# Optimization experiments

Hardware: AMD Instinct MI355X
Metric: run time of the kernel (lower is better)

The kernel has to match this reference:

```python
import jax, jax.numpy as jnp
import numpy as np

D_MODEL = 1024
D_K = 1024
B = 4
T = 2048

def setup_inputs() -> dict:
    key = jax.random.key(0)
    k_x, k_q, k_k, k_v = jax.random.split(key, 4)
    s = 1.0 / np.sqrt(D_MODEL)
    return {
        "x": jax.random.normal(k_x, (B, T, D_MODEL), dtype=jnp.float32),
        "Wq": jax.random.normal(k_q, (D_MODEL, D_K), dtype=jnp.float32) * s,
        "Wk": jax.random.normal(k_k, (D_MODEL, D_K), dtype=jnp.float32) * s,
        "Wv": jax.random.normal(k_v, (D_MODEL, D_K), dtype=jnp.float32) * s,
    }

def reference(x, Wq, Wk, Wv):
    # x: (B, T, d_model); Wq/Wk/Wv: (d_model, d_k)
    Q = jnp.einsum('btd,dk->btk', x, Wq)
    K = jnp.einsum('btd,dk->btk', x, Wk)
    V = jnp.einsum('btd,dk->btk', x, Wv)
    scale = 1.0 / jnp.sqrt(jnp.asarray(D_K, dtype=x.dtype))
    scores = jnp.einsum('bqk,bsk->bqs', Q, K) * scale  # (B, T, T)
    t = scores.shape[1]
    causal = jnp.triu(jnp.ones((t, t), dtype=bool), k=1)  # True above diagonal
    scores = jnp.where(causal[None, :, :], jnp.asarray(-jnp.inf, dtype=scores.dtype), scores)
    weights = jax.nn.softmax(scores, axis=-1)
    # dropout p=0.0 -> identity
    return jnp.einsum('bqs,bsk->bqk', weights, V)
```

## Files before the change

kernel.cpp:

```cpp
#include <hip/hip_runtime.h>
#include <cstdint>

typedef __attribute__((ext_vector_type(4))) float f32x4;
typedef __attribute__((ext_vector_type(8))) __bf16 bf16x8;
typedef __attribute__((ext_vector_type(8))) unsigned short u16x8;

__device__ __forceinline__ unsigned short f2bf(float f) {
    union { float f; unsigned u; } v; v.f = f;
    unsigned u = v.u + 0x7FFFu + ((v.u >> 16) & 1u);
    return (unsigned short)(u >> 16);
}
__device__ __forceinline__ float bf2f(unsigned short h) {
    union { unsigned u; float f; } v; v.u = ((unsigned)h) << 16;
    return v.f;
}

__device__ __forceinline__ void gld_lds16(const void* g, void* l) {
    auto gp = reinterpret_cast<const __attribute__((address_space(1))) unsigned int*>(
        reinterpret_cast<uintptr_t>(g));
    auto lp = reinterpret_cast<__attribute__((address_space(3))) unsigned int*>(
        reinterpret_cast<uintptr_t>(l));
    __builtin_amdgcn_global_load_lds(gp, lp, 16, 0, 0);
}

template<int BF16OUT>
__device__ __forceinline__ void gemm8(
    const unsigned short* __restrict__ A, int lda,
    const unsigned short* __restrict__ B, int ldb,
    void* __restrict__ C, int ldc,
    int ktiles,
    unsigned short* lA, unsigned short* lB)
{
    const int t = threadIdx.x;
    const int l = t & 63;
    const int w = t >> 6;
    const int wr = w >> 1, wc = w & 1;

    f32x4 acc[2][4];
#pragma unroll
    for (int i = 0; i < 2; ++i)
#pragma unroll
        for (int j = 0; j < 4; ++j)
#pragma unroll
            for (int e = 0; e < 4; ++e) acc[i][j][e] = 0.f;

    auto stage = [&](int p, int kt) {
        const int k0 = kt << 6;
#pragma unroll
        for (int i = 0; i < 2; ++i) {
            const int flat = t + (i << 9);
            const int row = flat >> 3;
            const int sc = (flat & 7) ^ (row & 7);
            gld_lds16(A + (size_t)row * lda + k0 + (sc << 3), lA + (p << 13) + (flat << 3));
            gld_lds16(B + (size_t)row * ldb + k0 + (sc << 3), lB + (p << 13) + (flat << 3));
        }
    };

    auto compute = [&](int p) {
#pragma unroll
        for (int kk = 0; kk < 2; ++kk) {
            bf16x8 af[2], bfr[4];
            const int c = (kk << 5) + ((l >> 4) << 3);
#pragma unroll
            for (int mf = 0; mf < 2; ++mf) {
                const int r = (wr << 5) + (mf << 4) + (l & 15);
                const int ad = (((r << 6) + c) ^ ((r & 7) << 3)) + (p << 13);
                af[mf] = *(const bf16x8*)(lA + ad);
            }
#pragma unroll
            for (int nf = 0; nf < 4; ++nf) {
                const int r = (wc << 6) + (nf << 4) + (l & 15);
                const int ad = (((r << 6) + c) ^ ((r & 7) << 3)) + (p << 13);
                bfr[nf] = *(const bf16x8*)(lB + ad);
            }
            __builtin_amdgcn_s_setprio(1);
#pragma unroll
            for (int mf = 0; mf < 2; ++mf)
#pragma unroll
                for (int nf = 0; nf < 4; ++nf)
                    acc[mf][nf] = __builtin_amdgcn_mfma_f32_16x16x32_bf16(
                        af[mf], bfr[nf], acc[mf][nf], 0, 0, 0);
            __builtin_amdgcn_s_setprio(0);
        }
    };

    stage(0, 0);
    __syncthreads();
    int p = 0;
    for (int kt = 0; kt < ktiles - 1; ++kt) {
        stage(p ^ 1, kt + 1);
        compute(p);
        __syncthreads();
        p ^= 1;
    }
    compute(p);

#pragma unroll
    for (int mf = 0; mf < 2; ++mf)
#pragma unroll
        for (int nf = 0; nf < 4; ++nf)
#pragma unroll
            for (int j = 0; j < 4; ++j) {
                const int row = (wr << 5) + (mf << 4) + ((l >> 4) << 2) + j;
                const int col = (wc << 6) + (nf << 4) + (l & 15);
                const float v = acc[mf][nf][j];
                if (BF16OUT)
                    ((unsigned short*)C)[(size_t)row * ldc + col] = f2bf(v);
                else
                    ((float*)C)[(size_t)row * ldc + col] = v;
            }
}

__global__ __launch_bounds__(512, 4) void k_gemm_qk(
    const unsigned short* __restrict__ xb, const unsigned short* __restrict__ wtqk,
    unsigned short* __restrict__ qk)
{
    __shared__ unsigned short lA[16384], lB[16384];
    gemm8<1>(xb + (size_t)blockIdx.y * 128 * 1024, 1024,
             wtqk + (size_t)blockIdx.x * 128 * 1024, 1024,
             qk + (size_t)blockIdx.y * 128 * 2048 + blockIdx.x * 128, 2048,
             16, lA, lB);
}

__global__ __launch_bounds__(512, 4) void k_gemm_vt(
    const unsigned short* __restrict__ wtv, const unsigned short* __restrict__ xb,
    unsigned short* __restrict__ vt)
{
    __shared__ unsigned short lA[16384], lB[16384];
    gemm8<1>(wtv + (size_t)blockIdx.y * 128 * 1024, 1024,
             xb + (size_t)blockIdx.x * 128 * 1024, 1024,
             vt + (size_t)blockIdx.y * 128 * 8192 + blockIdx.x * 128, 8192,
             16, lA, lB);
}

__global__ __launch_bounds__(512, 4) void k_scores(
    const unsigned short* __restrict__ qk, unsigned short* __restrict__ S)
{
    const int kt = blockIdx.x, qt = blockIdx.y, b = blockIdx.z;
    if (kt > qt) return;
    __shared__ unsigned short lA[16384], lB[16384];
    gemm8<1>(qk + ((size_t)b * 2048 + qt * 128) * 2048, 2048,
             qk + ((size_t)b * 2048 + kt * 128) * 2048 + 1024, 2048,
             S + (size_t)b * 4194304 + (size_t)qt * 128 * 2048 + kt * 128, 2048,
             16, lA, lB);
}

__global__ __launch_bounds__(512, 4) void k_pv(
    const unsigned short* __restrict__ P, const unsigned short* __restrict__ Vt,
    float* __restrict__ out)
{
    const int dn = blockIdx.x, pr = blockIdx.y, b = blockIdx.z;
    __shared__ unsigned short lA[16384], lB[16384];
    const int q1 = pr, q2 = 15 - pr;
    gemm8<0>(P + (size_t)b * 4194304 + (size_t)q1 * 128 * 2048, 2048,
             Vt + (size_t)dn * 128 * 8192 + b * 2048, 8192,
             out + ((size_t)b * 2048 + q1 * 128) * 1024 + dn * 128, 1024,
             (q1 + 1) * 2, lA, lB);
    __syncthreads();
    gemm8<0>(P + (size_t)b * 4194304 + (size_t)q2 * 128 * 2048, 2048,
             Vt + (size_t)dn * 128 * 8192 + b * 2048, 8192,
             out + ((size_t)b * 2048 + q2 * 128) * 1024 + dn * 128, 1024,
             (q2 + 1) * 2, lA, lB);
}

__global__ __launch_bounds__(256) void k_cast_bf16(
    const float* __restrict__ in, unsigned short* __restrict__ out, int n8)
{
    const int i = blockIdx.x * 256 + threadIdx.x;
    if (i >= n8) return;
    const float4* p = (const float4*)in + (size_t)i * 2;
    const float4 a = p[0], b = p[1];
    u16x8 r;
    r[0] = f2bf(a.x); r[1] = f2bf(a.y); r[2] = f2bf(a.z); r[3] = f2bf(a.w);
    r[4] = f2bf(b.x); r[5] = f2bf(b.y); r[6] = f2bf(b.z); r[7] = f2bf(b.w);
    *(u16x8*)(out + (size_t)i * 8) = r;
}

__global__ __launch_bounds__(256) void k_transpose3(
    const float* __restrict__ Wq, const float* __restrict__ Wk, const float* __restrict__ Wv,
    unsigned short* __restrict__ wtqk, unsigned short* __restrict__ wtv)
{
    __shared__ float tile[32][33];
    const int z = blockIdx.z;
    const float* in = (z == 0) ? Wq : (z == 1) ? Wk : Wv;
    unsigned short* out = (z < 2) ? (wtqk + (size_t)z * 1048576) : wtv;
    const float s = (z == 0) ? 0.03125f : 1.0f;
    const int bx = blockIdx.x * 32, by = blockIdx.y * 32;
    const int tx = threadIdx.x, ty = threadIdx.y;
    for (int r = ty; r < 32; r += 8)
        tile[r][tx] = in[(size_t)(by + r) * 1024 + bx + tx];
    __syncthreads();
    for (int r = ty; r < 32; r += 8)
        out[(size_t)(bx + r) * 1024 + by + tx] = f2bf(tile[tx][r] * s);
}

__global__ __launch_bounds__(256) void k_softmax(unsigned short* __restrict__ S)
{
    const int w = threadIdx.x >> 6, l = threadIdx.x & 63;
    const int r = blockIdx.x * 4 + w;
    const int b = r >> 11, lr = r & 2047;
    unsigned short* row = S + ((size_t)b << 22) + ((size_t)lr << 11);
    const int edge = ((lr >> 7) + 1) << 7;

    float v[32];
#pragma unroll
    for (int i = 0; i < 4; ++i) {
        const int c0 = (l << 3) + (i << 9);
        if (c0 < edge) {
            const u16x8 u = *(const u16x8*)(row + c0);
#pragma unroll
            for (int j = 0; j < 8; ++j)
                v[(i << 3) + j] = (c0 + j <= lr) ? bf2f(u[j]) : -3.0e38f;
        } else {
#pragma unroll
            for (int j = 0; j < 8; ++j) v[(i << 3) + j] = -3.0e38f;
        }
    }
    float m = v[0];
#pragma unroll
    for (int k = 1; k < 32; ++k) m = fmaxf(m, v[k]);
#pragma unroll
    for (int s = 32; s; s >>= 1) m = fmaxf(m, __shfl_xor(m, s, 64));
    float sum = 0.f;
#pragma unroll
    for (int k = 0; k < 32; ++k) { const float e = __expf(v[k] - m); v[k] = e; sum += e; }
#pragma unroll
    for (int s = 32; s; s >>= 1) sum += __shfl_xor(sum, s, 64);
    const float inv = 1.f / sum;
#pragma unroll
    for (int i = 0; i < 4; ++i) {
        const int c0 = (l << 3) + (i << 9);
        if (c0 < edge) {
            u16x8 o;
#pragma unroll
            for (int j = 0; j < 8; ++j) o[j] = f2bf(v[(i << 3) + j] * inv);
            *(u16x8*)(row + c0) = o;
        }
    }
}

extern "C" void kernel_launch(void* const* d_in, const int* in_sizes, int n_in,
                              void* d_out, int out_size, void* d_ws, size_t ws_size,
                              hipStream_t stream)
{
    (void)in_sizes; (void)n_in; (void)out_size; (void)ws_size;
    const float* x  = (const float*)d_in[0];
    const float* Wq = (const float*)d_in[1];
    const float* Wk = (const float*)d_in[2];
    const float* Wv = (const float*)d_in[3];
    float* out = (float*)d_out;

    char* w = (char*)d_ws;
    unsigned short* xb   = (unsigned short*)(w);
    unsigned short* wtqk = (unsigned short*)(w + 16777216);
    unsigned short* wtv  = (unsigned short*)(w + 20971520);
    unsigned short* QK   = (unsigned short*)(w + 23068672);
    unsigned short* Vt   = (unsigned short*)(w + 56623104);
    unsigned short* S    = (unsigned short*)(w + 73400320);

    k_cast_bf16<<<4096, 256, 0, stream>>>(x, xb, 1048576);
    k_transpose3<<<dim3(32, 32, 3), dim3(32, 8), 0, stream>>>(Wq, Wk, Wv, wtqk, wtv);

    k_gemm_qk<<<dim3(16, 64), 512, 0, stream>>>(xb, wtqk, QK);
    k_gemm_vt<<<dim3(64, 8), 512, 0, stream>>>(wtv, xb, Vt);

    k_scores <<<dim3(16, 16, 4), 512, 0, stream>>>(QK, S);
    k_softmax<<<2048, 256, 0, stream>>>(S);
    k_pv     <<<dim3(8, 8, 4), 512, 0, stream>>>(S, Vt, out);
}
```

Measured before the change: 228.8 us.

## Use 256x256 tiled GEMM with phased pipeline for projections and scores

Adds a 256x256-tile GEMM with 8 waves, each computing 128x64. It uses double-buffered LDS staged in halves and interleaves loads with MFMA phases separated by barriers. The Q/K and V^T projections are merged into one launch with an XCD-aware block remap. The causal scores kernel now launches only the lower-triangle 256-tiles instead of early-exiting blocks. The larger tiles cut global traffic per FLOP and launch overhead, at the cost of fewer blocks, lower occupancy (launch bound 2) and more register pressure from 32 accumulators.

```diff
diff --git a/kernel.cpp b/kernel.cpp
--- a/kernel.cpp
+++ b/kernel.cpp
@@ -21,6 +21,131 @@
     auto lp = reinterpret_cast<__attribute__((address_space(3))) unsigned int*>(
         reinterpret_cast<uintptr_t>(l));
     __builtin_amdgcn_global_load_lds(gp, lp, 16, 0, 0);
+}
+
+#define MFMA_BF16(a, b, c) __builtin_amdgcn_mfma_f32_16x16x32_bf16((a), (b), (c), 0, 0, 0)
+
+template<int BF16OUT>
+__device__ __forceinline__ void gemm256(
+    const unsigned short* __restrict__ A, int lda,
+    const unsigned short* __restrict__ B, int ldb,
+    void* __restrict__ C, int ldc,
+    int ktiles,
+    unsigned short* lA, unsigned short* lB)
+{
+    const int t = threadIdx.x;
+    const int l = t & 63;
+    const int w = t >> 6;
+    const int wm = w >> 2, wn = w & 3;
+
+    f32x4 acc[8][4];
+#pragma unroll
+    for (int i = 0; i < 8; ++i)
+#pragma unroll
+        for (int j = 0; j < 4; ++j)
+#pragma unroll
+            for (int e = 0; e < 4; ++e) acc[i][j][e] = 0.f;
+
+    auto stage = [&](const unsigned short* __restrict__ G, int ld, unsigned short* L,
+                     int p, int h, int kt) {
+        const int k0 = kt << 6;
+#pragma unroll
+        for (int i = 0; i < 2; ++i) {
+            const int flat = t + (i << 9);
+            const int row  = (h << 7) + (flat >> 3);
+            const int sc   = (flat & 7) ^ (row & 7);
+            gld_lds16(G + (size_t)row * ld + k0 + (sc << 3),
+                      L + (p << 14) + (h << 13) + (flat << 3));
+        }
+    };
+
+    auto rdA = [&](int p, int mf, int kk) -> bf16x8 {
+        const int r = (wm << 7) + (mf << 4) + (l & 15);
+        const int c = (kk << 5) + ((l >> 4) << 3);
+        const int ad = (((r << 6) + c) ^ ((r & 7) << 3)) + (p << 14);
+        return *(const bf16x8*)(lA + ad);
+    };
+    auto rdB = [&](int p, int nf, int kk) -> bf16x8 {
+        const int r = (wn << 6) + (nf << 4) + (l & 15);
+        const int c = (kk << 5) + ((l >> 4) << 3);
+        const int ad = (((r << 6) + c) ^ ((r & 7) << 3)) + (p << 14);
+        return *(const bf16x8*)(lB + ad);
+    };
+
+    const int kt1 = (ktiles > 1) ? 1 : 0;
+    stage(B, ldb, lB, 0, 0, 0); stage(B, ldb, lB, 0, 1, 0);
+    stage(A, lda, lA, 0, 0, 0); stage(A, lda, lA, 0, 1, 0);
+    stage(B, ldb, lB, 1, 0, kt1); stage(B, ldb, lB, 1, 1, kt1);
+    asm volatile("s_waitcnt vmcnt(4)" ::: "memory");
+    __builtin_amdgcn_s_barrier();
+
+#define MMA_PHASE(MF0, A00, A01, A10, A11)                                    \
+    __builtin_amdgcn_s_setprio(1);                                            \
+    _Pragma("unroll")                                                         \
+    for (int nf = 0; nf < 4; ++nf) {                                          \
+        acc[MF0][nf]     = MFMA_BF16(A00, bq[nf][0], acc[MF0][nf]);           \
+        acc[MF0][nf]     = MFMA_BF16(A01, bq[nf][1], acc[MF0][nf]);           \
+        acc[MF0 + 1][nf] = MFMA_BF16(A10, bq[nf][0], acc[MF0 + 1][nf]);       \
+        acc[MF0 + 1][nf] = MFMA_BF16(A11, bq[nf][1], acc[MF0 + 1][nf]);       \
+    }                                                                         \
+    __builtin_amdgcn_s_setprio(0);
+
+    for (int kt = 0; kt < ktiles; ++kt) {
+        const int p = kt & 1;
+        const int ktA = (kt + 1 < ktiles) ? kt + 1 : ktiles - 1;
+        const int ktB = (kt + 2 < ktiles) ? kt + 2 : ktiles - 1;
+
+        bf16x8 bq[4][2];
+#pragma unroll
+        for (int nf = 0; nf < 4; ++nf) {
+            bq[nf][0] = rdB(p, nf, 0);
+            bq[nf][1] = rdB(p, nf, 1);
+        }
+        bf16x8 a00 = rdA(p, 0, 0), a01 = rdA(p, 0, 1);
+        bf16x8 a10 = rdA(p, 1, 0), a11 = rdA(p, 1, 1);
+        stage(A, lda, lA, p ^ 1, 0, ktA);
+        __builtin_amdgcn_s_barrier();
+        MMA_PHASE(0, a00, a01, a10, a11)
+        __builtin_amdgcn_s_barrier();
+
+        a00 = rdA(p, 2, 0); a01 = rdA(p, 2, 1);
+        a10 = rdA(p, 3, 0); a11 = rdA(p, 3, 1);
+        stage(A, lda, lA, p ^ 1, 1, ktA);
+        stage(B, ldb, lB, p, 0, ktB);
+        __builtin_amdgcn_s_barrier();
+        MMA_PHASE(2, a00, a01, a10, a11)
+        __builtin_amdgcn_s_barrier();
+
+        a00 = rdA(p, 4, 0); a01 = rdA(p, 4, 1);
+        a10 = rdA(p, 5, 0); a11 = rdA(p, 5, 1);
+        stage(B, ldb, lB, p, 1, ktB);
+        __builtin_amdgcn_s_barrier();
+        MMA_PHASE(4, a00, a01, a10, a11)
+        __builtin_amdgcn_s_barrier();
+
+        a00 = rdA(p, 6, 0); a01 = rdA(p, 6, 1);
+        a10 = rdA(p, 7, 0); a11 = rdA(p, 7, 1);
+        __builtin_amdgcn_s_barrier();
+        MMA_PHASE(6, a00, a01, a10, a11)
+        asm volatile("s_waitcnt vmcnt(4)" ::: "memory");
+        __builtin_amdgcn_s_barrier();
+    }
+#undef MMA_PHASE
+
+#pragma unroll
+    for (int mf = 0; mf < 8; ++mf)
+#pragma unroll
+        for (int nf = 0; nf < 4; ++nf)
+#pragma unroll
+            for (int j = 0; j < 4; ++j) {
+                const int row = (wm << 7) + (mf << 4) + ((l >> 4) << 2) + j;
+                const int col = (wn << 6) + (nf << 4) + (l & 15);
+                const float v = acc[mf][nf][j];
+                if (BF16OUT)
+                    ((unsigned short*)C)[(size_t)row * ldc + col] = f2bf(v);
+                else
+                    ((float*)C)[(size_t)row * ldc + col] = v;
+            }
 }
 
 template<int BF16OUT>
@@ -78,8 +203,7 @@
             for (int mf = 0; mf < 2; ++mf)
 #pragma unroll
                 for (int nf = 0; nf < 4; ++nf)
-                    acc[mf][nf] = __builtin_amdgcn_mfma_f32_16x16x32_bf16(
-                        af[mf], bfr[nf], acc[mf][nf], 0, 0, 0);
+                    acc[mf][nf] = MFMA_BF16(af[mf], bfr[nf], acc[mf][nf]);
             __builtin_amdgcn_s_setprio(0);
         }
     };
@@ -111,38 +235,43 @@
             }
 }
 
-__global__ __launch_bounds__(512, 4) void k_gemm_qk(
+__global__ __launch_bounds__(512, 2) void k_proj256(
     const unsigned short* __restrict__ xb, const unsigned short* __restrict__ wtqk,
-    unsigned short* __restrict__ qk)
-{
-    __shared__ unsigned short lA[16384], lB[16384];
-    gemm8<1>(xb + (size_t)blockIdx.y * 128 * 1024, 1024,
-             wtqk + (size_t)blockIdx.x * 128 * 1024, 1024,
-             qk + (size_t)blockIdx.y * 128 * 2048 + blockIdx.x * 128, 2048,
-             16, lA, lB);
-}
-
-__global__ __launch_bounds__(512, 4) void k_gemm_vt(
-    const unsigned short* __restrict__ wtv, const unsigned short* __restrict__ xb,
-    unsigned short* __restrict__ vt)
-{
-    __shared__ unsigned short lA[16384], lB[16384];
-    gemm8<1>(wtv + (size_t)blockIdx.y * 128 * 1024, 1024,
-             xb + (size_t)blockIdx.x * 128 * 1024, 1024,
-             vt + (size_t)blockIdx.y * 128 * 8192 + blockIdx.x * 128, 8192,
-             16, lA, lB);
-}
-
-__global__ __launch_bounds__(512, 4) void k_scores(
+    const unsigned short* __restrict__ wtv,
+    unsigned short* __restrict__ qk, unsigned short* __restrict__ vt)
+{
+    __shared__ unsigned short lA[32768], lB[32768];
+    const int h = blockIdx.x;
+    const int lgc = (h & 7) * 48 + (h >> 3);
+    if (lgc < 256) {
+        const int by = lgc >> 3, bx = lgc & 7;
+        gemm256<1>(xb + (size_t)by * 256 * 1024, 1024,
+                   wtqk + (size_t)bx * 256 * 1024, 1024,
+                   qk + (size_t)by * 256 * 2048 + bx * 256, 2048,
+                   16, lA, lB);
+    } else {
+        const int l2 = lgc - 256;
+        const int dn = l2 & 3, tn = l2 >> 2;
+        gemm256<1>(wtv + (size_t)dn * 256 * 1024, 1024,
+                   xb + (size_t)tn * 256 * 1024, 1024,
+                   vt + (size_t)dn * 256 * 8192 + tn * 256, 8192,
+                   16, lA, lB);
+    }
+}
+
+__global__ __launch_bounds__(512, 2) void k_scores256(
     const unsigned short* __restrict__ qk, unsigned short* __restrict__ S)
 {
-    const int kt = blockIdx.x, qt = blockIdx.y, b = blockIdx.z;
-    if (kt > qt) return;
-    __shared__ unsigned short lA[16384], lB[16384];
-    gemm8<1>(qk + ((size_t)b * 2048 + qt * 128) * 2048, 2048,
-             qk + ((size_t)b * 2048 + kt * 128) * 2048 + 1024, 2048,
-             S + (size_t)b * 4194304 + (size_t)qt * 128 * 2048 + kt * 128, 2048,
-             16, lA, lB);
+    __shared__ unsigned short lA[32768], lB[32768];
+    const int b = blockIdx.z;
+    const int tidx = blockIdx.x;
+    int qt2 = 0;
+    while ((qt2 + 1) * (qt2 + 2) / 2 <= tidx) ++qt2;
+    const int kt2 = tidx - qt2 * (qt2 + 1) / 2;
+    gemm256<1>(qk + ((size_t)b * 2048 + qt2 * 256) * 2048, 2048,
+               qk + ((size_t)b * 2048 + kt2 * 256) * 2048 + 1024, 2048,
+               S + (size_t)b * 4194304 + (size_t)qt2 * 256 * 2048 + kt2 * 256, 2048,
+               16, lA, lB);
 }
 
 __global__ __launch_bounds__(512, 4) void k_pv(
@@ -261,10 +390,9 @@
     k_cast_bf16<<<4096, 256, 0, stream>>>(x, xb, 1048576);
     k_transpose3<<<dim3(32, 32, 3), dim3(32, 8), 0, stream>>>(Wq, Wk, Wv, wtqk, wtv);
 
-    k_gemm_qk<<<dim3(16, 64), 512, 0, stream>>>(xb, wtqk, QK);
-    k_gemm_vt<<<dim3(64, 8), 512, 0, stream>>>(wtv, xb, Vt);
-
-    k_scores <<<dim3(16, 16, 4), 512, 0, stream>>>(QK, S);
+    k_proj256<<<384, 512, 0, stream>>>(xb, wtqk, wtv, QK, Vt);
+
+    k_scores256<<<dim3(36, 1, 4), 512, 0, stream>>>(QK, S);
     k_softmax<<<2048, 256, 0, stream>>>(S);
-    k_pv     <<<dim3(8, 8, 4), 512, 0, stream>>>(S, Vt, out);
-}
+    k_pv<<<dim3(8, 8, 4), 512, 0, stream>>>(S, Vt, out);
+}
```

Measured after the change: 229.3 us. No clear change (+0.2%).
